# Kernel tuning notes

Hardware: AMD Instinct MI355X
Metric: run time of the kernel (lower is better)

The kernel has to match this reference:

```python
import jax, jax.numpy as jnp
import numpy as np

B, IN_UNITS, IN_CH, NUM_UNITS, UNIT_SIZE = 32, 16, 2048, 16, 64
NUM_ITERS = 2


def setup_inputs() -> dict:
    key = jax.random.key(0)
    k1, k2 = jax.random.split(key)
    x = jax.random.normal(k1, (B, IN_UNITS, IN_CH), dtype=jnp.float32)
    W = jax.random.normal(k2, (1, IN_CH, NUM_UNITS, UNIT_SIZE, IN_UNITS), dtype=jnp.float32)
    return {"x": x, "W": W}


def squash(s):
    # torch code sums squared magnitude over dim=2 (the num_units axis) with keepdim
    mag_sq = jnp.sum(s * s, axis=2, keepdims=True)
    mag = jnp.sqrt(mag_sq)
    return mag_sq / (1.0 + mag_sq) * (s / mag)


def reference(x, W):
    # x: (B, in_units, in_channels) -> (B, in_channels, in_units)
    xt = jnp.swapaxes(x, 1, 2)
    # u_hat[b,i,j,k] = sum_u W[0,i,j,k,u] * xt[b,i,u]  -> (B, IC, NU, US)
    u_hat = jnp.einsum('ijku,biu->bijk', W[0], xt)
    b_ij = jnp.zeros((1, IN_CH, NUM_UNITS, 1), dtype=x.dtype)
    v_j = None
    for _ in range(NUM_ITERS):
        # softmax over a singleton trailing dim -> all ones (faithful to source)
        c_ij = jax.nn.softmax(b_ij, axis=-1)  # (1, IC, NU, 1), broadcasts over batch
        s_j = jnp.sum(c_ij[None, ..., 0][0][None].squeeze(0) * 0 + c_ij * u_hat, axis=1, keepdims=True) if False else jnp.sum(c_ij * u_hat, axis=1, keepdims=True)  # (B,1,NU,US)
        v_j = squash(s_j)  # (B,1,NU,US)
        # agreement: <u_hat, v_j> over unit_size, broadcast v_j over in_channels
        u_vj1 = jnp.einsum('bijk,bljk->bij', u_hat, v_j)  # (B, IC, NU)
        u_vj1 = jnp.mean(u_vj1, axis=0, keepdims=True)[..., None]  # (1, IC, NU, 1)
        b_ij = b_ij + u_vj1
    return v_j[:, 0, :, :]  # (B, num_units, unit_size)
```

## Files before the change

kernel.cpp:

```cpp
#include <hip/hip_runtime.h>
#include <hip/hip_bf16.h>


#define B_SZ   32
#define IC     2048
#define NJ     16
#define NK     64
#define SOUT   (B_SZ*NJ*NK)
#define KSTEPS 1024
#define KSPLIT 128
#define SPW    (KSTEPS/KSPLIT)

typedef float v4f __attribute__((ext_vector_type(4)));
typedef short v8s __attribute__((ext_vector_type(8)));
typedef unsigned int v4u __attribute__((ext_vector_type(4)));

static __device__ inline ushort f2bf(float f) {
    uint32_t u = __float_as_uint(f);
    u += 0x7FFFu + ((u >> 16) & 1u);
    return (ushort)(u >> 16);
}

static __device__ inline uint packbf(float f0, float f1) {
    uint u0 = __float_as_uint(f0) + 0x8000u;
    uint u1 = __float_as_uint(f1) + 0x8000u;
    return __builtin_amdgcn_perm(u1, u0, 0x07060302u);
}

__global__ __launch_bounds__(256)
void caps_xprep(const float* __restrict__ x, ushort* __restrict__ xb) {
    int gid  = blockIdx.x * 256 + threadIdx.x;
    int lane = gid & 63;
    int mt   = (gid >> 6) & 1;
    int step = gid >> 7;
    int q    = lane >> 4;
    int b    = mt * 16 + (lane & 15);
    int i    = 2 * step + (q >> 1);
    int u0   = (q & 1) * 8;

    const float* xp = x + (size_t)b * (16 * IC) + (size_t)u0 * IC + i;
    ushort tmp[8];
    #pragma unroll
    for (int jj = 0; jj < 8; ++jj)
        tmp[jj] = f2bf(xp[(size_t)jj * IC]);
    *(v8s*)(xb + (size_t)gid * 8) = *(const v8s*)tmp;
}

__global__ __launch_bounds__(256, 6)
void caps_mfma(const ushort* __restrict__ xb, const float* __restrict__ W,
               float* __restrict__ part) {
    const int tid   = threadIdx.x;
    const int wv    = tid >> 6;
    const int lane  = tid & 63;
    const int j     = blockIdx.x;
    const int split = blockIdx.y;
    const int n     = lane & 15;
    const int q     = lane >> 4;
    const int step0 = split * SPW;

    v4f acc0 = {0.f, 0.f, 0.f, 0.f};
    v4f acc1 = {0.f, 0.f, 0.f, 0.f};

    const float*  wp = W + (size_t)(2 * step0 + (q >> 1)) * 16384
                         + (size_t)j * 1024 + (size_t)(wv * 16 + n) * 16 + (q & 1) * 8;
    const ushort* xp = xb + (size_t)step0 * 1024 + (size_t)lane * 8;

    float4 w0 = *(const float4*)(wp);
    float4 w1 = *(const float4*)(wp + 4);
    v8s    a0 = *(const v8s*)(xp);
    v8s    a1 = *(const v8s*)(xp + 512);

    #pragma unroll
    for (int s = 0; s < SPW - 1; ++s) {
        wp += 2 * 16384;
        xp += 1024;
        float4 nw0 = *(const float4*)(wp);
        float4 nw1 = *(const float4*)(wp + 4);
        v8s    na0 = *(const v8s*)(xp);
        v8s    na1 = *(const v8s*)(xp + 512);

        v4u pk;
        pk.x = packbf(w0.x, w0.y); pk.y = packbf(w0.z, w0.w);
        pk.z = packbf(w1.x, w1.y); pk.w = packbf(w1.z, w1.w);
        v8s bb = *(v8s*)&pk;
        acc0 = __builtin_amdgcn_mfma_f32_16x16x32_bf16(a0, bb, acc0, 0, 0, 0);
        acc1 = __builtin_amdgcn_mfma_f32_16x16x32_bf16(a1, bb, acc1, 0, 0, 0);

        w0 = nw0; w1 = nw1; a0 = na0; a1 = na1;
    }
    {
        v4u pk;
        pk.x = packbf(w0.x, w0.y); pk.y = packbf(w0.z, w0.w);
        pk.z = packbf(w1.x, w1.y); pk.w = packbf(w1.z, w1.w);
        v8s bb = *(v8s*)&pk;
        acc0 = __builtin_amdgcn_mfma_f32_16x16x32_bf16(a0, bb, acc0, 0, 0, 0);
        acc1 = __builtin_amdgcn_mfma_f32_16x16x32_bf16(a1, bb, acc1, 0, 0, 0);
    }

    float* pp = part + (size_t)split * SOUT + (size_t)j * NK + wv * 16 + n;
    #pragma unroll
    for (int r = 0; r < 4; ++r) {
        int m = q * 4 + r;
        pp[(size_t)m * 1024]        = acc0[r];
        pp[(size_t)(m + 16) * 1024] = acc1[r];
    }
}

__global__ __launch_bounds__(256)
void caps_finish(const float* __restrict__ part, float* __restrict__ out) {
    __shared__ float ls[256];
    const int blk = blockIdx.x;
    const int b   = blk >> 2;
    const int k0  = (blk & 3) * 16;
    const int t   = threadIdx.x;
    const int jj  = t >> 4;
    const int kc  = t & 15;
    const size_t idx = (size_t)b * 1024 + (size_t)jj * NK + k0 + kc;

    float s = 0.0f;
    #pragma unroll 8
    for (int sp = 0; sp < KSPLIT; ++sp)
        s += part[(size_t)sp * SOUT + idx];
    ls[t] = s;
    __syncthreads();

    float msq = 0.0f;
    #pragma unroll
    for (int j2 = 0; j2 < NJ; ++j2) {
        float v = ls[j2 * 16 + kc];
        msq += v * v;
    }
    float mag = sqrtf(msq);
    out[idx] = s * (mag / (1.0f + msq));
}

extern "C" void kernel_launch(void* const* d_in, const int* in_sizes, int n_in,
                              void* d_out, int out_size, void* d_ws, size_t ws_size,
                              hipStream_t stream) {
    const float* x = (const float*)d_in[0];
    const float* W = (const float*)d_in[1];
    float* out  = (float*)d_out;

    float*  part = (float*)d_ws;
    ushort* xb   = (ushort*)(part + (size_t)KSPLIT * SOUT);

    caps_xprep <<<512,               256, 0, stream>>>(x, xb);
    caps_mfma  <<<dim3(16, KSPLIT),  256, 0, stream>>>(xb, W, part);
    caps_finish<<<128,               256, 0, stream>>>(part, out);
}
```

Measured before the change: 208.4 us.

## Halve K-split and batch loads four steps deep in MFMA loop

Halves the number of K-split partitions, so each block covers 16 steps and the finish kernel reduces half as many partials. The software-pipelined one-ahead prefetch loop is replaced by a loop that issues four steps of W and x loads before the MFMAs, which gives more memory-level parallelism per wave. The occupancy hint in launch bounds is removed. The grid has half as many blocks (1024) and each thread holds more registers, so fewer waves may be resident to hide latency.

New measurement: 205.6 us. About the same (-1.3%).

```diff
diff --git a/kernel.cpp b/kernel.cpp
--- a/kernel.cpp
+++ b/kernel.cpp
@@ -8,8 +8,9 @@
 #define NK     64
 #define SOUT   (B_SZ*NJ*NK)
 #define KSTEPS 1024
-#define KSPLIT 128
+#define KSPLIT 64
 #define SPW    (KSTEPS/KSPLIT)
+#define BATCH  4
 
 typedef float v4f __attribute__((ext_vector_type(4)));
 typedef short v8s __attribute__((ext_vector_type(8)));
@@ -46,7 +47,7 @@
     *(v8s*)(xb + (size_t)gid * 8) = *(const v8s*)tmp;
 }
 
-__global__ __launch_bounds__(256, 6)
+__global__ __launch_bounds__(256)
 void caps_mfma(const ushort* __restrict__ xb, const float* __restrict__ W,
                float* __restrict__ part) {
     const int tid   = threadIdx.x;
@@ -65,36 +66,30 @@
                          + (size_t)j * 1024 + (size_t)(wv * 16 + n) * 16 + (q & 1) * 8;
     const ushort* xp = xb + (size_t)step0 * 1024 + (size_t)lane * 8;
 
-    float4 w0 = *(const float4*)(wp);
-    float4 w1 = *(const float4*)(wp + 4);
-    v8s    a0 = *(const v8s*)(xp);
-    v8s    a1 = *(const v8s*)(xp + 512);
-
-    #pragma unroll
-    for (int s = 0; s < SPW - 1; ++s) {
-        wp += 2 * 16384;
-        xp += 1024;
-        float4 nw0 = *(const float4*)(wp);
-        float4 nw1 = *(const float4*)(wp + 4);
-        v8s    na0 = *(const v8s*)(xp);
-        v8s    na1 = *(const v8s*)(xp + 512);
-
-        v4u pk;
-        pk.x = packbf(w0.x, w0.y); pk.y = packbf(w0.z, w0.w);
-        pk.z = packbf(w1.x, w1.y); pk.w = packbf(w1.z, w1.w);
-        v8s bb = *(v8s*)&pk;
-        acc0 = __builtin_amdgcn_mfma_f32_16x16x32_bf16(a0, bb, acc0, 0, 0, 0);
-        acc1 = __builtin_amdgcn_mfma_f32_16x16x32_bf16(a1, bb, acc1, 0, 0, 0);
-
-        w0 = nw0; w1 = nw1; a0 = na0; a1 = na1;
-    }
-    {
-        v4u pk;
-        pk.x = packbf(w0.x, w0.y); pk.y = packbf(w0.z, w0.w);
-        pk.z = packbf(w1.x, w1.y); pk.w = packbf(w1.z, w1.w);
-        v8s bb = *(v8s*)&pk;
-        acc0 = __builtin_amdgcn_mfma_f32_16x16x32_bf16(a0, bb, acc0, 0, 0, 0);
-        acc1 = __builtin_amdgcn_mfma_f32_16x16x32_bf16(a1, bb, acc1, 0, 0, 0);
+    #pragma unroll 1
+    for (int ss = 0; ss < SPW / BATCH; ++ss) {
+        float4 wb0[BATCH], wb1[BATCH];
+        v8s    ab0[BATCH], ab1[BATCH];
+        #pragma unroll
+        for (int t = 0; t < BATCH; ++t) {
+            const float*  wpt = wp + (size_t)t * (2 * 16384);
+            const ushort* xpt = xp + (size_t)t * 1024;
+            wb0[t] = *(const float4*)(wpt);
+            wb1[t] = *(const float4*)(wpt + 4);
+            ab0[t] = *(const v8s*)(xpt);
+            ab1[t] = *(const v8s*)(xpt + 512);
+        }
+        #pragma unroll
+        for (int t = 0; t < BATCH; ++t) {
+            v4u pk;
+            pk.x = packbf(wb0[t].x, wb0[t].y); pk.y = packbf(wb0[t].z, wb0[t].w);
+            pk.z = packbf(wb1[t].x, wb1[t].y); pk.w = packbf(wb1[t].z, wb1[t].w);
+            v8s bb = *(v8s*)&pk;
+            acc0 = __builtin_amdgcn_mfma_f32_16x16x32_bf16(ab0[t], bb, acc0, 0, 0, 0);
+            acc1 = __builtin_amdgcn_mfma_f32_16x16x32_bf16(ab1[t], bb, acc1, 0, 0, 0);
+        }
+        wp += (size_t)BATCH * 2 * 16384;
+        xp += (size_t)BATCH * 1024;
     }
 
     float* pp = part + (size_t)split * SOUT + (size_t)j * NK + wv * 16 + n;
```
